# Performance work log

Measured on AMD Instinct MI355X. Metric: run time of the kernel, lower is better.

The kernel has to match this reference:

```python
import jax, jax.numpy as jnp
import numpy as np

DEPTH = 256
SEQ = 394
EMB = 300


def _branch(x_nch, W, b, n):
    # W: [depth, n*EMB], flatten order of paragraph[i:i+n,:].flatten() is (time, emb)
    k = W.reshape(DEPTH, n, EMB).transpose(0, 2, 1)  # OIH: [depth, EMB, n]
    y = jax.lax.conv_general_dilated(
        x_nch, k, window_strides=(1,), padding='VALID',
        dimension_numbers=('NCH', 'OIH', 'NCH'))  # [B, depth, SEQ-n+1]
    # original loop only covers windows i = 0 .. SEQ-n-1 (SEQ-n windows)
    y = y[:, :, :SEQ - n] + b  # b: [depth, 1] broadcasts over time
    # running max starts at 0 and relu clamps >= 0; outer relu is a no-op
    return jnp.max(jax.nn.relu(y), axis=-1)  # [B, depth]


def setup_inputs() -> dict:
    key = jax.random.key(0)
    ks = jax.random.split(key, 7)
    inp = {
        'input': jax.random.normal(ks[0], (64, SEQ, EMB), dtype=jnp.float32),
        'W1': jax.random.normal(ks[1], (DEPTH, 3 * EMB), dtype=jnp.float32),
        'W2': jax.random.normal(ks[2], (DEPTH, 4 * EMB), dtype=jnp.float32),
        'W3': jax.random.normal(ks[3], (DEPTH, 5 * EMB), dtype=jnp.float32),
        'b1': jax.random.normal(ks[4], (DEPTH, 1), dtype=jnp.float32),
        'b2': jax.random.normal(ks[5], (DEPTH, 1), dtype=jnp.float32),
        'b3': jax.random.normal(ks[6], (DEPTH, 1), dtype=jnp.float32),
    }
    return inp


def reference(input, W1, W2, W3, b1, b2, b3):
    x = input.transpose(0, 2, 1)  # [B, EMB, SEQ] (NCH)
    o1 = _branch(x, W1, b1, 3)
    o2 = _branch(x, W2, b2, 4)
    o3 = _branch(x, W3, b3, 5)
    return jnp.concatenate([o1, o2, o3], axis=1)  # [B, 3*depth]
```

## Files before the change

### kernel.cpp

```cpp
#include <hip/hip_runtime.h>
#include <hip/hip_bf16.h>

#define SEQ 394
#define EMB 300
#define EMBP 312
#define NROWS (64 * SEQ)
#define XPTOT ((long)NROWS * EMBP)
#define NCHT 118
#define CBE0 29
#define CBE1 68
#define XELEM 41472

typedef __attribute__((ext_vector_type(8))) short short8;
typedef __attribute__((ext_vector_type(4))) float f32x4;

__device__ __forceinline__ unsigned short f2b(float f) {
    unsigned u = __float_as_uint(f);
    u += 0x7FFFu + ((u >> 16) & 1u);
    return (unsigned short)(u >> 16);
}

__device__ __forceinline__ void gload_lds16(const void* g, void* l) {
    __builtin_amdgcn_global_load_lds(
        (const __attribute__((address_space(1))) void*)g,
        (__attribute__((address_space(3))) void*)l, 16, 0, 0);
}


__global__ __launch_bounds__(256)
void pack_x_kernel(const float* __restrict__ x, unsigned short* __restrict__ xp)
{
    long q = (long)blockIdx.x * 256 + threadIdx.x;
    int row = (int)(q / 78);
    int c4  = ((int)(q - (long)row * 78)) * 4;
    ushort4 u;
    if (c4 < 300) {
        float4 v = *(const float4*)(x + (long)row * 300 + c4);
        u = make_ushort4(f2b(v.x), f2b(v.y), f2b(v.z), f2b(v.w));
    } else {
        u = make_ushort4(0, 0, 0, 0);
    }
    *(ushort4*)(xp + q * 4) = u;
}

__global__ __launch_bounds__(256)
void pack_w_kernel(const float* __restrict__ W1, const float* __restrict__ W2,
                   const float* __restrict__ W3, unsigned short* __restrict__ wb)
{
    int G = blockIdx.x * 256 + threadIdx.x;
    int l  = G & 63;
    int g  = (G >> 6) & 15;
    int c  = G >> 10;
    const float* Wg; int n, cb;
    if (c <= CBE0)      { Wg = W1; n = 3; cb = 0;        }
    else if (c <= CBE1) { Wg = W2; n = 4; cb = CBE0 + 1; }
    else                { Wg = W3; n = 5; cb = CBE1 + 1; }
    const int K = n * 300;
    const int f = g * 16 + (l & 15);
    const int kl = (c - cb) * 32 + (l >> 4) * 8;
    unsigned short v[8];
#pragma unroll
    for (int j = 0; j < 8; ++j) {
        int kk = kl + j;
        int r  = kk / EMBP;
        int e  = kk - r * EMBP;
        v[j] = (r < n && e < 300) ? f2b(Wg[(long)f * K + r * 300 + e]) : (unsigned short)0;
    }
    unsigned short* dst = wb + (long)G * 8;
    *(ushort4*)dst       = make_ushort4(v[0], v[1], v[2], v[3]);
    *(ushort4*)(dst + 4) = make_ushort4(v[4], v[5], v[6], v[7]);
}


__global__ __launch_bounds__(1024, 1)
void convgemm_kernel(const unsigned short* __restrict__ xp,
                     const unsigned short* __restrict__ wb,
                     const float* __restrict__ b1, const float* __restrict__ b2,
                     const float* __restrict__ b3,
                     float* __restrict__ out)
{
    __shared__ unsigned short X[XELEM];

    const int tid  = threadIdx.x;
    const int lane = tid & 63;
    const int wid  = tid >> 6;
    const int wfs  = wid >> 1;
    const int ws   = wid & 1;
    const int lr   = lane & 15, lg = lane >> 4;
    const int b    = blockIdx.x >> 2;
    const int ti   = blockIdx.x & 3;
    const int woff = (ti == 0) ? 0 : (ti == 1) ? 88 : (ti == 2) ? 176 : 263;

    {
        const long xbase = ((long)b * SEQ + woff) * EMBP;
        const long slim  = XPTOT - 8;
#pragma unroll
        for (int rd = 0; rd < 6; ++rd) {
            int gbase = rd * 1024 + wid * 64;
            if (gbase < 5184) {
                long se = xbase + (long)(gbase + lane) * 8;
                if (se > slim) se = slim;
                gload_lds16(xp + se, &X[gbase * 8]);
            }
        }
    }
    __syncthreads();

    const unsigned short* wp0 = wb + ((long)(wfs * 2) * 64 + lane) * 8;
    auto LDW = [&](int c, short8 w[2]) {
        const short8* p = (const short8*)(wp0 + (long)c * 8192);
        w[0] = p[0];
        w[1] = p[64];
    };

    const unsigned short* xr = &X[(ws * 64 + lr) * EMBP + lg * 8];
    auto RDBX = [&](int ko, short8 bx[4]) {
        bx[0] = *(const short8*)(xr + ko);
        bx[1] = *(const short8*)(xr + ko + 16 * EMBP);
        bx[2] = *(const short8*)(xr + ko + 32 * EMBP);
        bx[3] = *(const short8*)(xr + ko + 48 * EMBP);
    };

    f32x4 acc[2][4];
#pragma unroll
    for (int i = 0; i < 2; ++i)
#pragma unroll
        for (int j = 0; j < 4; ++j)
            acc[i][j] = (f32x4)0.0f;

    auto MFMA8 = [&](short8 w[2], short8 bx[4]) {
#pragma unroll
        for (int mi = 0; mi < 2; ++mi)
#pragma unroll
            for (int ni = 0; ni < 4; ++ni)
                acc[mi][ni] = __builtin_amdgcn_mfma_f32_16x16x32_bf16(w[mi], bx[ni], acc[mi][ni], 0, 0, 0);
    };

    auto EPI = [&](int br) {
        const float* bg = (br == 0) ? b1 : (br == 1) ? b2 : b3;
        const int Nw = 391 - br;
        const int ob = b * 768 + br * 256;
#pragma unroll
        for (int mi = 0; mi < 2; ++mi) {
#pragma unroll
            for (int r = 0; r < 4; ++r) {
                const int d = wfs * 32 + mi * 16 + lg * 4 + r;
                const float bv = bg[d];
                float m = 0.f;
#pragma unroll
                for (int ni = 0; ni < 4; ++ni) {
                    int w = woff + ws * 64 + ni * 16 + lr;
                    float v = fmaxf(acc[mi][ni][r] + bv, 0.f);
                    if (w >= Nw) v = 0.f;
                    m = fmaxf(m, v);
                }
#pragma unroll
                for (int off = 1; off < 16; off <<= 1)
                    m = fmaxf(m, __shfl_xor(m, off));
                if (lr == 0)
                    atomicMax((int*)(out + ob + d), __float_as_int(m));
            }
        }
#pragma unroll
        for (int i = 0; i < 2; ++i)
#pragma unroll
            for (int j = 0; j < 4; ++j)
                acc[i][j] = (f32x4)0.0f;
    };

    auto KOF = [](int t) {
        return (t >= 69) ? (t - 69) * 32 : (t >= 30) ? (t - 30) * 32 : t * 32;
    };

    short8 wA[2], wB[2], bxA[4], bxB[4];
    LDW(0, wA); LDW(1, wB);
    RDBX(0, bxA);

    for (int c = 0; c < NCHT; c += 2) {
        RDBX(KOF(c + 1), bxB);
        MFMA8(wA, bxA);
        {
            int t = (c + 2 < NCHT) ? c + 2 : NCHT - 1;
            LDW(t, wA);
        }
        if (c == CBE1) EPI(1);

        {
            int t = (c + 2 < NCHT) ? c + 2 : NCHT - 1;
            RDBX(KOF(t), bxA);
        }
        MFMA8(wB, bxB);
        {
            int t = (c + 3 < NCHT) ? c + 3 : NCHT - 1;
            LDW(t, wB);
        }
        if (c + 1 == CBE0) EPI(0);
        if (c + 1 == NCHT - 1) EPI(2);
    }
}


__device__ __forceinline__ void load_chunk(const float* __restrict__ Wg,
                                           const float* __restrict__ xb,
                                           int K, int dbase, int i0, int k0, int tid,
                                           float4 wv[4], float4 xv[4])
{
#pragma unroll
    for (int i = 0; i < 4; ++i) {
        int fi  = tid + (i << 8);
        int row = fi >> 3;
        int c4  = (fi & 7) << 2;
        int col = k0 + c4;
        if (col < K)
            wv[i] = *(const float4*)(Wg + (long)(dbase + row) * K + col);
        else
            wv[i] = make_float4(0.f, 0.f, 0.f, 0.f);
        int off = (i0 + row) * EMB + col;
        int lim = SEQ * EMB - 4;
        if (off > lim) off = lim;
        xv[i] = *(const float4*)(xb + off);
    }
}

__device__ __forceinline__ void write_chunk(unsigned short (*Wb)[40],
                                            unsigned short (*Xb)[40],
                                            int tid, const float4 wv[4], const float4 xv[4])
{
#pragma unroll
    for (int i = 0; i < 4; ++i) {
        int fi  = tid + (i << 8);
        int row = fi >> 3;
        int c4  = (fi & 7) << 2;
        *(ushort4*)&Wb[row][c4] = make_ushort4(f2b(wv[i].x), f2b(wv[i].y), f2b(wv[i].z), f2b(wv[i].w));
        *(ushort4*)&Xb[row][c4] = make_ushort4(f2b(xv[i].x), f2b(xv[i].y), f2b(xv[i].z), f2b(xv[i].w));
    }
}

__global__ __launch_bounds__(256, 2)
void convmax_fallback(const float* __restrict__ x,
                      const float* __restrict__ W1, const float* __restrict__ W2,
                      const float* __restrict__ W3,
                      const float* __restrict__ b1, const float* __restrict__ b2,
                      const float* __restrict__ b3,
                      float* __restrict__ out)
{
    const int br = blockIdx.z;
    const int K  = (br == 0) ? 900 : (br == 1) ? 1200 : 1500;
    const int Nw = SEQ - 3 - br;
    const float* Wg = (br == 0) ? W1 : (br == 1) ? W2 : W3;
    const float* bg = (br == 0) ? b1 : (br == 1) ? b2 : b3;
    const int b  = blockIdx.x;
    const int mt = blockIdx.y >> 2;
    const int nt = blockIdx.y & 3;
    const int dbase = mt * 128;
    const int i0    = nt * 128;
    const float* xb = x + b * (SEQ * EMB);
    const int nch = (K + 31) >> 5;

    __shared__ unsigned short Wl[2][128][40];
    __shared__ unsigned short Xl[2][128][40];

    const int tid  = threadIdx.x;
    const int lane = tid & 63;
    const int wid  = tid >> 6;
    const int wr = wid >> 1, wc = wid & 1;
    const int lr = lane & 15, lg = lane >> 4;

    f32x4 acc[4][4];
#pragma unroll
    for (int i = 0; i < 4; ++i)
#pragma unroll
        for (int j = 0; j < 4; ++j)
            acc[i][j] = (f32x4)0.0f;

    {
        float4 wv[4], xv[4];
        load_chunk(Wg, xb, K, dbase, i0, 0, tid, wv, xv);
        write_chunk(Wl[0], Xl[0], tid, wv, xv);
    }
    __syncthreads();

    for (int c = 0; c < nch; ++c) {
        const int cur = c & 1;
        float4 wv[4], xv[4];
        const bool pf = (c + 1 < nch);
        if (pf) load_chunk(Wg, xb, K, dbase, i0, (c + 1) << 5, tid, wv, xv);

        short8 af[4], bfr[4];
#pragma unroll
        for (int mi = 0; mi < 4; ++mi)
            af[mi] = *(const short8*)&Wl[cur][wr * 64 + mi * 16 + lr][lg * 8];
#pragma unroll
        for (int ni = 0; ni < 4; ++ni)
            bfr[ni] = *(const short8*)&Xl[cur][wc * 64 + ni * 16 + lr][lg * 8];
#pragma unroll
        for (int mi = 0; mi < 4; ++mi)
#pragma unroll
            for (int ni = 0; ni < 4; ++ni)
                acc[mi][ni] = __builtin_amdgcn_mfma_f32_16x16x32_bf16(af[mi], bfr[ni], acc[mi][ni], 0, 0, 0);

        if (pf) write_chunk(Wl[cur ^ 1], Xl[cur ^ 1], tid, wv, xv);
        __syncthreads();
    }

    const int ob = b * 768 + br * 256;
#pragma unroll
    for (int mi = 0; mi < 4; ++mi) {
#pragma unroll
        for (int rI = 0; rI < 4; ++rI) {
            const int d = dbase + wr * 64 + mi * 16 + lg * 4 + rI;
            const float bv = bg[d];
            float m = 0.f;
#pragma unroll
            for (int ni = 0; ni < 4; ++ni) {
                int win = i0 + wc * 64 + ni * 16 + lr;
                float v = acc[mi][ni][rI] + bv;
                v = fmaxf(v, 0.f);
                if (win >= Nw) v = 0.f;
                m = fmaxf(m, v);
            }
#pragma unroll
            for (int off = 1; off < 16; off <<= 1)
                m = fmaxf(m, __shfl_xor(m, off));
            if (lr == 0)
                atomicMax((int*)(out + ob + d), __float_as_int(m));
        }
    }
}


extern "C" void kernel_launch(void* const* d_in, const int* in_sizes, int n_in,
                              void* d_out, int out_size, void* d_ws, size_t ws_size,
                              hipStream_t stream) {
    const float* x  = (const float*)d_in[0];
    const float* W1 = (const float*)d_in[1];
    const float* W2 = (const float*)d_in[2];
    const float* W3 = (const float*)d_in[3];
    const float* b1 = (const float*)d_in[4];
    const float* b2 = (const float*)d_in[5];
    const float* b3 = (const float*)d_in[6];
    float* out = (float*)d_out;

    hipMemsetAsync(d_out, 0, (size_t)out_size * sizeof(float), stream);

    const long WBTOT = (long)NCHT * 8192;
    const size_t need = (size_t)(XPTOT + WBTOT) * 2;

    if (ws_size >= need) {
        unsigned short* xp = (unsigned short*)d_ws;
        unsigned short* wbb = xp + XPTOT;

        pack_x_kernel<<<7683, 256, 0, stream>>>(x, xp);
        pack_w_kernel<<<472, 256, 0, stream>>>(W1, W2, W3, wbb);
        convgemm_kernel<<<256, 1024, 0, stream>>>(xp, wbb, b1, b2, b3, out);
    } else {
        dim3 grid(64, 8, 3);
        convmax_fallback<<<grid, 256, 0, stream>>>(x, W1, W2, W3, b1, b2, b3, out);
    }
}
```

Baseline: 86.34 us.

## Share LDS activation fragments across branches with dual accumulators

The main MFMA loop now processes the k=4 and k=5 branch chunks for the same K offset together. Each LDS read of the activation fragments feeds two weight sets into two accumulator arrays, and the loop then finishes the k=5 tail and runs the k=3 branch separately. This cuts LDS reads for the overlapping K range roughly in half. In exchange it doubles the accumulator registers and holds four weight fragment sets live, which may raise VGPR pressure and reduce occupancy. It also removes the single-buffered double-pipelined bx prefetch, so LDS latency is less hidden.

```diff
diff --git a/kernel.cpp b/kernel.cpp
--- a/kernel.cpp
+++ b/kernel.cpp
@@ -107,28 +107,21 @@
     __syncthreads();
 
     const unsigned short* wp0 = wb + ((long)(wfs * 2) * 64 + lane) * 8;
-    auto LDW = [&](int c, short8 w[2]) {
+    auto LDW = [&](int c, short8 (&w)[2]) {
         const short8* p = (const short8*)(wp0 + (long)c * 8192);
         w[0] = p[0];
         w[1] = p[64];
     };
 
     const unsigned short* xr = &X[(ws * 64 + lr) * EMBP + lg * 8];
-    auto RDBX = [&](int ko, short8 bx[4]) {
+    auto RDBX = [&](int ko, short8 (&bx)[4]) {
         bx[0] = *(const short8*)(xr + ko);
         bx[1] = *(const short8*)(xr + ko + 16 * EMBP);
         bx[2] = *(const short8*)(xr + ko + 32 * EMBP);
         bx[3] = *(const short8*)(xr + ko + 48 * EMBP);
     };
 
-    f32x4 acc[2][4];
-#pragma unroll
-    for (int i = 0; i < 2; ++i)
-#pragma unroll
-        for (int j = 0; j < 4; ++j)
-            acc[i][j] = (f32x4)0.0f;
-
-    auto MFMA8 = [&](short8 w[2], short8 bx[4]) {
+    auto MFMA8 = [&](const short8 (&w)[2], const short8 (&bx)[4], f32x4 (&acc)[2][4]) {
 #pragma unroll
         for (int mi = 0; mi < 2; ++mi)
 #pragma unroll
@@ -136,7 +129,7 @@
                 acc[mi][ni] = __builtin_amdgcn_mfma_f32_16x16x32_bf16(w[mi], bx[ni], acc[mi][ni], 0, 0, 0);
     };
 
-    auto EPI = [&](int br) {
+    auto EPI = [&](int br, f32x4 (&acc)[2][4]) {
         const float* bg = (br == 0) ? b1 : (br == 1) ? b2 : b3;
         const int Nw = 391 - br;
         const int ob = b * 768 + br * 256;
@@ -168,35 +161,60 @@
                 acc[i][j] = (f32x4)0.0f;
     };
 
-    auto KOF = [](int t) {
-        return (t >= 69) ? (t - 69) * 32 : (t >= 30) ? (t - 30) * 32 : t * 32;
-    };
-
-    short8 wA[2], wB[2], bxA[4], bxB[4];
-    LDW(0, wA); LDW(1, wB);
-    RDBX(0, bxA);
-
-    for (int c = 0; c < NCHT; c += 2) {
-        RDBX(KOF(c + 1), bxB);
-        MFMA8(wA, bxA);
-        {
-            int t = (c + 2 < NCHT) ? c + 2 : NCHT - 1;
-            LDW(t, wA);
+    f32x4 accA[2][4], accB[2][4];
+#pragma unroll
+    for (int i = 0; i < 2; ++i)
+#pragma unroll
+        for (int j = 0; j < 4; ++j) {
+            accA[i][j] = (f32x4)0.0f;
+            accB[i][j] = (f32x4)0.0f;
         }
-        if (c == CBE1) EPI(1);
-
-        {
-            int t = (c + 2 < NCHT) ? c + 2 : NCHT - 1;
-            RDBX(KOF(t), bxA);
-        }
-        MFMA8(wB, bxB);
-        {
-            int t = (c + 3 < NCHT) ? c + 3 : NCHT - 1;
-            LDW(t, wB);
-        }
-        if (c + 1 == CBE0) EPI(0);
-        if (c + 1 == NCHT - 1) EPI(2);
-    }
+
+    short8 w1A[2], w1B[2], w2A[2], w2B[2], bx[4];
+
+    LDW(30, w1A); LDW(69, w2A);
+    LDW(31, w1B); LDW(70, w2B);
+    for (int j = 0; j < 38; j += 2) {
+        RDBX(j * 32, bx);
+        MFMA8(w1A, bx, accA);
+        MFMA8(w2A, bx, accB);
+        { int t = (j + 2 < 39) ? j + 2 : 38; LDW(30 + t, w1A); LDW(69 + t, w2A); }
+
+        RDBX((j + 1) * 32, bx);
+        MFMA8(w1B, bx, accA);
+        MFMA8(w2B, bx, accB);
+        { int t = (j + 3 < 39) ? j + 3 : 38; LDW(30 + t, w1B); LDW(69 + t, w2B); }
+    }
+    RDBX(38 * 32, bx);
+    MFMA8(w1A, bx, accA);
+    MFMA8(w2A, bx, accB);
+
+    LDW(69 + 39, w2A); LDW(69 + 40, w2B);
+    EPI(1, accA);
+
+    for (int t = 0; t < 10; t += 2) {
+        RDBX((39 + t) * 32, bx);
+        MFMA8(w2A, bx, accB);
+        { int u = (41 + t < 49) ? 41 + t : 48; LDW(69 + u, w2A); }
+
+        RDBX((40 + t) * 32, bx);
+        MFMA8(w2B, bx, accB);
+        { int u = (42 + t < 49) ? 42 + t : 48; LDW(69 + u, w2B); }
+    }
+
+    LDW(0, w1A); LDW(1, w1B);
+    EPI(2, accB);
+
+    for (int j = 0; j < 30; j += 2) {
+        RDBX(j * 32, bx);
+        MFMA8(w1A, bx, accA);
+        { int t = (j + 2 < 30) ? j + 2 : 29; LDW(t, w1A); }
+
+        RDBX((j + 1) * 32, bx);
+        MFMA8(w1B, bx, accA);
+        { int t = (j + 3 < 30) ? j + 3 : 29; LDW(t, w1B); }
+    }
+    EPI(0, accA);
 }
 
 
```

Result: no change. 85.00 us (-1.6%).
